# Optimization experiments

Measured on AMD Instinct MI355X. Metric: run time of the kernel, lower is better.

The kernel has to match this reference:

```python
import jax, jax.numpy as jnp
import numpy as np

N = 100_000      # nodes
E = 1_250_000    # edges (avg degree ~12.5)
D_IN, D_H, D_OUT = 64, 64, 64


def setup_inputs() -> dict:
    key = jax.random.key(0)
    ks = jax.random.split(key, 7)
    x = jax.random.normal(ks[0], (N, D_IN), dtype=jnp.float32)
    edge_index = jax.random.randint(ks[1], (2, E), 0, N, dtype=jnp.int32)
    edge_weight = jax.random.uniform(ks[2], (E,), dtype=jnp.float32)
    # GCNConv linear weights: PyG lin stores [out, in], applied as x @ W.T; bias added after aggregation.
    W1 = jax.random.normal(ks[3], (D_H, D_IN), dtype=jnp.float32) * (1.0 / np.sqrt(D_IN))
    b1 = jax.random.normal(ks[4], (D_H,), dtype=jnp.float32) * 0.01
    W2 = jax.random.normal(ks[5], (D_OUT, D_H), dtype=jnp.float32) * (1.0 / np.sqrt(D_H))
    b2 = jax.random.normal(ks[6], (D_OUT,), dtype=jnp.float32) * 0.01
    return {"x": x, "edge_index": edge_index, "edge_weight": edge_weight,
            "W1": W1, "b1": b1, "W2": W2, "b2": b2}


def _gcn_conv(x, src, dst, w, W, b, n_nodes):
    # PyG GCNConv: add self-loops (weight 1), symmetric normalization, linear, scatter-add, +bias.
    deg = jax.ops.segment_sum(w, dst, num_segments=n_nodes) + 1.0  # +1 from self-loop
    dis = jnp.where(deg > 0, jax.lax.rsqrt(deg), 0.0)              # deg^{-1/2}
    coef = dis[src] * w * dis[dst]                                 # per-edge norm, [E]
    h = x @ W.T                                                    # [N, out]
    agg = jax.ops.segment_sum(h[src] * coef[:, None], dst, num_segments=n_nodes)
    agg = agg + h * (dis * dis)[:, None]                           # self-loop: dis_i * 1 * dis_i
    return agg + b


def reference(x, edge_index, edge_weight, W1, b1, W2, b2):
    n = x.shape[0]
    src, dst = edge_index[0], edge_index[1]
    h = _gcn_conv(x, src, dst, edge_weight, W1, b1, n)
    h = jax.nn.relu(h)
    # dropout p=0.0 -> identity
    return _gcn_conv(h, src, dst, edge_weight, W2, b2, n)
```

## Files before the change

kernel.cpp:

```cpp
#include <hip/hip_runtime.h>


typedef unsigned int u32;
typedef unsigned short u16;

#define NBKT 256
#define LSH 9
#define BNODES 512
#define CAP 8192
#define SRCBITS 17
#define SRCMASK ((1u << SRCBITS) - 1u)

__device__ inline u16 f2bf(float f) {
  u32 u = __float_as_uint(f);
  u32 r = u + 0x7FFFu + ((u >> 16) & 1u);
  return (u16)(r >> 16);
}
__device__ inline float bf_lo(u32 p) { return __uint_as_float(p << 16); }
__device__ inline float bf_hi(u32 p) { return __uint_as_float(p & 0xFFFF0000u); }

__device__ inline u32 blockscan256_excl(u32 val, u32* wsum) {
  int lane = threadIdx.x & 63, wv = threadIdx.x >> 6;
  u32 inc = val;
  #pragma unroll
  for (int d = 1; d < 64; d <<= 1) {
    u32 t = __shfl_up(inc, d);
    if (lane >= d) inc += t;
  }
  if (lane == 63) wsum[wv] = inc;
  __syncthreads();
  u32 off = 0;
  #pragma unroll
  for (int i = 0; i < 4; ++i) if (i < wv) off += wsum[i];
  return off + inc - val;
}

__global__ void k_deg_bin(const int* __restrict__ ei, const float* __restrict__ w,
                          float* __restrict__ deg, u32* __restrict__ bucket_cnt,
                          u32* __restrict__ blockbase, int E, int chunk) {
  __shared__ u32 hist[NBKT];
  if (threadIdx.x < NBKT) hist[threadIdx.x] = 0u;
  __syncthreads();
  int e0 = blockIdx.x * chunk;
  int e1 = min(E, e0 + chunk);
  for (int e = e0 + (threadIdx.x << 1); e < e1; e += 512) {
    if (e + 1 < e1) {
      int2 dd = *(const int2*)(ei + E + e);
      float2 wv = *(const float2*)(w + e);
      atomicAdd(&hist[dd.x >> LSH], 1u);
      atomicAdd(&hist[dd.y >> LSH], 1u);
      atomicAdd(&deg[dd.x], wv.x);
      atomicAdd(&deg[dd.y], wv.y);
    } else {
      int d = ei[E + e];
      atomicAdd(&hist[d >> LSH], 1u);
      atomicAdd(&deg[d], w[e]);
    }
  }
  __syncthreads();
  if (threadIdx.x < NBKT)
    blockbase[threadIdx.x * 256 + blockIdx.x] =
        atomicAdd(&bucket_cnt[threadIdx.x], hist[threadIdx.x]);
}

__global__ __launch_bounds__(256, 4) void k_scatter_gemm(
    const int* __restrict__ ei, const float* __restrict__ w,
    const u32* __restrict__ blockbase,
    uint2* __restrict__ bucketed,
    const float* __restrict__ X, const float* __restrict__ W,
    const float* __restrict__ deg, u16* __restrict__ H, int N, int E, int chunk) {
  __shared__ float Wt[64 * 65];
  __shared__ float Xs[16 * 64];
  __shared__ u32 base[NBKT];
  int tid = threadIdx.x;
  if ((int)blockIdx.x < 256) {
    if (tid < NBKT)
      base[tid] = (u32)tid * CAP + blockbase[tid * 256 + blockIdx.x];
    __syncthreads();
    int e0 = blockIdx.x * chunk, e1 = min(E, e0 + chunk);
    for (int e = e0 + (tid << 1); e < e1; e += 512) {
      if (e + 1 < e1) {
        int2 ss = *(const int2*)(ei + e);
        int2 dd = *(const int2*)(ei + E + e);
        float2 wv = *(const float2*)(w + e);
        u32 p0 = atomicAdd(&base[dd.x >> LSH], 1u);
        u32 p1 = atomicAdd(&base[dd.y >> LSH], 1u);
        bucketed[p0] = make_uint2((u32)ss.x | ((u32)(dd.x & (BNODES - 1)) << SRCBITS),
                                  __float_as_uint(wv.x));
        bucketed[p1] = make_uint2((u32)ss.y | ((u32)(dd.y & (BNODES - 1)) << SRCBITS),
                                  __float_as_uint(wv.y));
      } else {
        int s = ei[e], d = ei[E + e];
        u32 pos = atomicAdd(&base[d >> LSH], 1u);
        bucketed[pos] = make_uint2((u32)s | ((u32)(d & (BNODES - 1)) << SRCBITS),
                                   __float_as_uint(w[e]));
      }
    }
    return;
  }
  int row0 = ((int)blockIdx.x - 256) * 16;
  if (row0 >= N) return;
  for (int i = tid; i < 4096; i += 256) Wt[(i & 63) * 65 + (i >> 6)] = W[i];
  {
    const float4* xsrc = (const float4*)(X + (size_t)row0 * 64);
    if (row0 + 16 <= N) {
      ((float4*)Xs)[tid] = xsrc[tid];
    } else {
      int r = tid >> 4;
      ((float4*)Xs)[tid] = (row0 + r < N) ? xsrc[tid]
                                          : make_float4(0.f, 0.f, 0.f, 0.f);
    }
  }
  __syncthreads();
  int lane = tid & 63, wv4 = tid >> 6;
  int rbase = wv4 * 4;
  float a0 = 0.f, a1 = 0.f, a2 = 0.f, a3 = 0.f;
  #pragma unroll 4
  for (int k4 = 0; k4 < 16; ++k4) {
    int k = k4 << 2;
    float w0 = Wt[k * 65 + lane], w1 = Wt[(k + 1) * 65 + lane];
    float w2 = Wt[(k + 2) * 65 + lane], w3 = Wt[(k + 3) * 65 + lane];
    float4 xa = *(const float4*)&Xs[(rbase + 0) * 64 + k];
    float4 xb = *(const float4*)&Xs[(rbase + 1) * 64 + k];
    float4 xc = *(const float4*)&Xs[(rbase + 2) * 64 + k];
    float4 xd = *(const float4*)&Xs[(rbase + 3) * 64 + k];
    a0 = fmaf(xa.x, w0, fmaf(xa.y, w1, fmaf(xa.z, w2, fmaf(xa.w, w3, a0))));
    a1 = fmaf(xb.x, w0, fmaf(xb.y, w1, fmaf(xb.z, w2, fmaf(xb.w, w3, a1))));
    a2 = fmaf(xc.x, w0, fmaf(xc.y, w1, fmaf(xc.z, w2, fmaf(xc.w, w3, a2))));
    a3 = fmaf(xd.x, w0, fmaf(xd.y, w1, fmaf(xd.z, w2, fmaf(xd.w, w3, a3))));
  }
  int row = row0 + rbase;
  if (row + 3 < N) {
    float dv0 = rsqrtf(1.f + deg[row]);
    float dv1 = rsqrtf(1.f + deg[row + 1]);
    float dv2 = rsqrtf(1.f + deg[row + 2]);
    float dv3 = rsqrtf(1.f + deg[row + 3]);
    H[(size_t)row * 64 + lane]       = f2bf(a0 * dv0);
    H[(size_t)(row + 1) * 64 + lane] = f2bf(a1 * dv1);
    H[(size_t)(row + 2) * 64 + lane] = f2bf(a2 * dv2);
    H[(size_t)(row + 3) * 64 + lane] = f2bf(a3 * dv3);
  } else {
    if (row < N)     H[(size_t)row * 64 + lane]       = f2bf(a0 * rsqrtf(1.f + deg[row]));
    if (row + 1 < N) H[(size_t)(row + 1) * 64 + lane] = f2bf(a1 * rsqrtf(1.f + deg[row + 1]));
    if (row + 2 < N) H[(size_t)(row + 2) * 64 + lane] = f2bf(a2 * rsqrtf(1.f + deg[row + 2]));
    if (row + 3 < N) H[(size_t)(row + 3) * 64 + lane] = f2bf(a3 * rsqrtf(1.f + deg[row + 3]));
  }
}

__global__ void k_statsfill(const uint2* __restrict__ bucketed,
                            const u32* __restrict__ bucket_cnt,
                            const float* __restrict__ deg,
                            int4* __restrict__ info, int2* __restrict__ csr, int N) {
  __shared__ u32 hist[BNODES];
  __shared__ u32 cur[BNODES];
  __shared__ u32 wsum[4];
  int b = blockIdx.x, tid = threadIdx.x;
  for (int i = tid; i < BNODES; i += 256) hist[i] = 0u;
  __syncthreads();
  u32 s0 = (u32)b * CAP, s1 = s0 + bucket_cnt[b];
  for (u32 p = s0 + tid; p < s1; p += 256)
    atomicAdd(&hist[bucketed[p].x >> SRCBITS], 1u);
  __syncthreads();
  u32 c0 = hist[2 * tid], c1 = hist[2 * tid + 1];
  u32 excl = blockscan256_excl(c0 + c1, wsum);
  cur[2 * tid] = excl;
  cur[2 * tid + 1] = excl + c0;
  int n0 = b * BNODES + 2 * tid;
  if (n0 < N) {
    float d0 = rsqrtf(1.f + deg[n0]);
    info[n0] = make_int4((int)(s0 + excl), (int)c0, __float_as_int(d0), 0);
  }
  if (n0 + 1 < N) {
    float d1 = rsqrtf(1.f + deg[n0 + 1]);
    info[n0 + 1] = make_int4((int)(s0 + excl + c0), (int)c1, __float_as_int(d1), 0);
  }
  __syncthreads();
  for (u32 p = s0 + tid; p < s1; p += 256) {
    uint2 ed = bucketed[p];
    u32 pos = atomicAdd(&cur[ed.x >> SRCBITS], 1u);
    csr[s0 + pos] = make_int2((int)(ed.x & SRCMASK), (int)ed.y);
  }
}

__global__ __launch_bounds__(256, 6) void k_agg_gemm(
    const u16* __restrict__ H, const int4* __restrict__ info,
    const int2* __restrict__ csr, const float* __restrict__ bias,
    const float* __restrict__ W2, const float* __restrict__ deg,
    u16* __restrict__ H2, int N) {
  __shared__ float Wt[64 * 65];
  __shared__ float Ys[16 * 64];
  int tid = threadIdx.x;
  for (int i = tid; i < 4096; i += 256) Wt[(i & 63) * 65 + (i >> 6)] = W2[i];
  int node = blockIdx.x * 16 + (tid >> 4);
  int fid = (tid & 15) << 2;
  bool valid = node < N;
  int4 nfo = valid ? info[node] : make_int4(0, 0, 0, 0);
  int s0 = nfo.x, n = nfo.y;
  float d = __int_as_float(nfo.z);
  uint2 hs = valid ? *(const uint2*)(H + (size_t)node * 64 + fid)
                   : make_uint2(0u, 0u);
  float4 b4 = *(const float4*)(bias + fid);
  float4 acc = make_float4(0.f, 0.f, 0.f, 0.f);
  int nm1 = n - 1;
  for (int base = 0; base < n; base += 4) {
    int q1 = min(base + 1, nm1);
    int q2 = min(base + 2, nm1), q3 = min(base + 3, nm1);
    int2 c0 = csr[s0 + base];
    int2 c1 = csr[s0 + q1];
    int2 c2 = csr[s0 + q2];
    int2 c3 = csr[s0 + q3];
    uint2 h0 = *(const uint2*)(H + (size_t)c0.x * 64 + fid);
    uint2 h1 = *(const uint2*)(H + (size_t)c1.x * 64 + fid);
    uint2 h2 = *(const uint2*)(H + (size_t)c2.x * 64 + fid);
    uint2 h3 = *(const uint2*)(H + (size_t)c3.x * 64 + fid);
    float f0 = __int_as_float(c0.y);
    float f1 = (base + 1 < n) ? __int_as_float(c1.y) : 0.f;
    float f2 = (base + 2 < n) ? __int_as_float(c2.y) : 0.f;
    float f3 = (base + 3 < n) ? __int_as_float(c3.y) : 0.f;
    acc.x = fmaf(bf_lo(h0.x), f0, acc.x); acc.y = fmaf(bf_hi(h0.x), f0, acc.y);
    acc.z = fmaf(bf_lo(h0.y), f0, acc.z); acc.w = fmaf(bf_hi(h0.y), f0, acc.w);
    acc.x = fmaf(bf_lo(h1.x), f1, acc.x); acc.y = fmaf(bf_hi(h1.x), f1, acc.y);
    acc.z = fmaf(bf_lo(h1.y), f1, acc.z); acc.w = fmaf(bf_hi(h1.y), f1, acc.w);
    acc.x = fmaf(bf_lo(h2.x), f2, acc.x); acc.y = fmaf(bf_hi(h2.x), f2, acc.y);
    acc.z = fmaf(bf_lo(h2.y), f2, acc.z); acc.w = fmaf(bf_hi(h2.y), f2, acc.w);
    acc.x = fmaf(bf_lo(h3.x), f3, acc.x); acc.y = fmaf(bf_hi(h3.x), f3, acc.y);
    acc.z = fmaf(bf_lo(h3.y), f3, acc.z); acc.w = fmaf(bf_hi(h3.y), f3, acc.w);
  }
  if (valid) {
    acc.x = fmaxf((acc.x + bf_lo(hs.x)) * d + b4.x, 0.f);
    acc.y = fmaxf((acc.y + bf_hi(hs.x)) * d + b4.y, 0.f);
    acc.z = fmaxf((acc.z + bf_lo(hs.y)) * d + b4.z, 0.f);
    acc.w = fmaxf((acc.w + bf_hi(hs.y)) * d + b4.w, 0.f);
  } else {
    acc = make_float4(0.f, 0.f, 0.f, 0.f);
  }
  *(float4*)&Ys[(tid >> 4) * 64 + fid] = acc;
  __syncthreads();
  int lane = tid & 63, wv = tid >> 6;
  int rbase = wv * 4;
  int row0 = blockIdx.x * 16;
  float a0 = 0.f, a1 = 0.f, a2 = 0.f, a3 = 0.f;
  #pragma unroll 4
  for (int k4 = 0; k4 < 16; ++k4) {
    int k = k4 << 2;
    float w0 = Wt[k * 65 + lane], w1 = Wt[(k + 1) * 65 + lane];
    float w2 = Wt[(k + 2) * 65 + lane], w3 = Wt[(k + 3) * 65 + lane];
    float4 xa = *(const float4*)&Ys[(rbase + 0) * 64 + k];
    float4 xb = *(const float4*)&Ys[(rbase + 1) * 64 + k];
    float4 xc = *(const float4*)&Ys[(rbase + 2) * 64 + k];
    float4 xd = *(const float4*)&Ys[(rbase + 3) * 64 + k];
    a0 = fmaf(xa.x, w0, fmaf(xa.y, w1, fmaf(xa.z, w2, fmaf(xa.w, w3, a0))));
    a1 = fmaf(xb.x, w0, fmaf(xb.y, w1, fmaf(xb.z, w2, fmaf(xb.w, w3, a1))));
    a2 = fmaf(xc.x, w0, fmaf(xc.y, w1, fmaf(xc.z, w2, fmaf(xc.w, w3, a2))));
    a3 = fmaf(xd.x, w0, fmaf(xd.y, w1, fmaf(xd.z, w2, fmaf(xd.w, w3, a3))));
  }
  int row = row0 + rbase;
  if (row + 3 < N) {
    float dv0 = rsqrtf(1.f + deg[row]);
    float dv1 = rsqrtf(1.f + deg[row + 1]);
    float dv2 = rsqrtf(1.f + deg[row + 2]);
    float dv3 = rsqrtf(1.f + deg[row + 3]);
    H2[(size_t)row * 64 + lane]       = f2bf(a0 * dv0);
    H2[(size_t)(row + 1) * 64 + lane] = f2bf(a1 * dv1);
    H2[(size_t)(row + 2) * 64 + lane] = f2bf(a2 * dv2);
    H2[(size_t)(row + 3) * 64 + lane] = f2bf(a3 * dv3);
  } else {
    if (row < N)     H2[(size_t)row * 64 + lane]       = f2bf(a0 * rsqrtf(1.f + deg[row]));
    if (row + 1 < N) H2[(size_t)(row + 1) * 64 + lane] = f2bf(a1 * rsqrtf(1.f + deg[row + 1]));
    if (row + 2 < N) H2[(size_t)(row + 2) * 64 + lane] = f2bf(a2 * rsqrtf(1.f + deg[row + 2]));
    if (row + 3 < N) H2[(size_t)(row + 3) * 64 + lane] = f2bf(a3 * rsqrtf(1.f + deg[row + 3]));
  }
}

__global__ __launch_bounds__(256, 8) void k_aggregate2(
    const u16* __restrict__ H, const int4* __restrict__ info,
    const int2* __restrict__ csr, const float* __restrict__ bias,
    float* __restrict__ Y, int N) {
  int tid = threadIdx.x;
  int node = blockIdx.x * 16 + (tid >> 4);
  int fid = (tid & 15) << 2;
  bool valid = node < N;
  int4 nfo = valid ? info[node] : make_int4(0, 0, 0, 0);
  int s0 = nfo.x, n = nfo.y;
  float d = __int_as_float(nfo.z);
  uint2 hs = valid ? *(const uint2*)(H + (size_t)node * 64 + fid)
                   : make_uint2(0u, 0u);
  float4 b4 = *(const float4*)(bias + fid);
  float4 acc = make_float4(0.f, 0.f, 0.f, 0.f);
  int nm1 = n - 1;
  for (int base = 0; base < n; base += 4) {
    int q1 = min(base + 1, nm1);
    int q2 = min(base + 2, nm1), q3 = min(base + 3, nm1);
    int2 c0 = csr[s0 + base];
    int2 c1 = csr[s0 + q1];
    int2 c2 = csr[s0 + q2];
    int2 c3 = csr[s0 + q3];
    uint2 h0 = *(const uint2*)(H + (size_t)c0.x * 64 + fid);
    uint2 h1 = *(const uint2*)(H + (size_t)c1.x * 64 + fid);
    uint2 h2 = *(const uint2*)(H + (size_t)c2.x * 64 + fid);
    uint2 h3 = *(const uint2*)(H + (size_t)c3.x * 64 + fid);
    float f0 = __int_as_float(c0.y);
    float f1 = (base + 1 < n) ? __int_as_float(c1.y) : 0.f;
    float f2 = (base + 2 < n) ? __int_as_float(c2.y) : 0.f;
    float f3 = (base + 3 < n) ? __int_as_float(c3.y) : 0.f;
    acc.x = fmaf(bf_lo(h0.x), f0, acc.x); acc.y = fmaf(bf_hi(h0.x), f0, acc.y);
    acc.z = fmaf(bf_lo(h0.y), f0, acc.z); acc.w = fmaf(bf_hi(h0.y), f0, acc.w);
    acc.x = fmaf(bf_lo(h1.x), f1, acc.x); acc.y = fmaf(bf_hi(h1.x), f1, acc.y);
    acc.z = fmaf(bf_lo(h1.y), f1, acc.z); acc.w = fmaf(bf_hi(h1.y), f1, acc.w);
    acc.x = fmaf(bf_lo(h2.x), f2, acc.x); acc.y = fmaf(bf_hi(h2.x), f2, acc.y);
    acc.z = fmaf(bf_lo(h2.y), f2, acc.z); acc.w = fmaf(bf_hi(h2.y), f2, acc.w);
    acc.x = fmaf(bf_lo(h3.x), f3, acc.x); acc.y = fmaf(bf_hi(h3.x), f3, acc.y);
    acc.z = fmaf(bf_lo(h3.y), f3, acc.z); acc.w = fmaf(bf_hi(h3.y), f3, acc.w);
  }
  if (valid) {
    acc.x = (acc.x + bf_lo(hs.x)) * d + b4.x;
    acc.y = (acc.y + bf_hi(hs.x)) * d + b4.y;
    acc.z = (acc.z + bf_lo(hs.y)) * d + b4.z;
    acc.w = (acc.w + bf_hi(hs.y)) * d + b4.w;
    *(float4*)(Y + (size_t)node * 64 + fid) = acc;
  }
}

extern "C" void kernel_launch(void* const* d_in, const int* in_sizes, int n_in,
                              void* d_out, int out_size, void* d_ws, size_t ws_size,
                              hipStream_t stream) {
  const float* x  = (const float*)d_in[0];
  const int*   ei = (const int*)d_in[1];
  const float* w  = (const float*)d_in[2];
  const float* W1 = (const float*)d_in[3];
  const float* b1 = (const float*)d_in[4];
  const float* W2 = (const float*)d_in[5];
  const float* b2 = (const float*)d_in[6];
  const int N = in_sizes[0] / 64;
  const int E = in_sizes[2];

  char* ws = (char*)d_ws;
  size_t off = 0;
  auto alloc = [&](size_t bytes) -> char* {
    char* p = ws + off;
    off = (off + bytes + 255) & ~(size_t)255;
    return p;
  };
  float* deg          = (float*)alloc((size_t)N * 4);
  u32*   bucket_cnt   = (u32*)  alloc((size_t)NBKT * 4);
  size_t zero_bytes   = (size_t)((char*)(bucket_cnt + NBKT) - (char*)deg);
  u32*   blockbase    = (u32*)  alloc((size_t)NBKT * 256 * 4);
  uint2* bucketed     = (uint2*)alloc((size_t)NBKT * CAP * 8);
  int2*  csr          = (int2*) alloc((size_t)NBKT * CAP * 8);
  int4*  info         = (int4*) alloc((size_t)N * 16);
  u16*   h1           = (u16*)  alloc((size_t)N * 64 * 2);
  u16*   h2           = (u16*)  alloc((size_t)N * 64 * 2);

  const int chunk = ((E + 511) / 512) * 2;
  const int nbG = (N + 15) / 16;
  const int nbA = (N + 15) / 16;
  const int nbB = (N + BNODES - 1) >> LSH;

  hipMemsetAsync(deg, 0, zero_bytes, stream);
  k_deg_bin<<<256, 256, 0, stream>>>(ei, w, deg, bucket_cnt, blockbase, E, chunk);
  k_scatter_gemm<<<256 + nbG, 256, 0, stream>>>(ei, w, blockbase, bucketed,
                                                x, W1, deg, h1, N, E, chunk);
  k_statsfill<<<nbB, 256, 0, stream>>>(bucketed, bucket_cnt, deg, info, csr, N);
  k_agg_gemm<<<nbA, 256, 0, stream>>>(h1, info, csr, b1, W2, deg, h2, N);
  k_aggregate2<<<nbA, 256, 0, stream>>>(h2, info, csr, b2, (float*)d_out, N);
}
```

Measured before the change: 286.5 us.

## Compute degrees in LDS during bucket fill instead of global float atomics

Removes the 1.25M global float atomicAdds on deg from the binning kernel. The weighted degree is now accumulated in the per-bucket statsfill kernel with LDS integer atomics, packing a count (high 8 bits) and a fixed-point weight sum (low 24 bits) into one word. Because dis is not known until statsfill, the first GEMM writes unscaled H, and statsfill then rescales its 512 rows of H in place, adding an extra read-modify-write pass over h1. The fixed-point packing limits precision and overflows if a node has 256 or more incoming edges or a weight sum of 64 or more.

```diff
diff --git a/kernel.cpp b/kernel.cpp
--- a/kernel.cpp
+++ b/kernel.cpp
@@ -35,9 +35,8 @@
   return off + inc - val;
 }
 
-__global__ void k_deg_bin(const int* __restrict__ ei, const float* __restrict__ w,
-                          float* __restrict__ deg, u32* __restrict__ bucket_cnt,
-                          u32* __restrict__ blockbase, int E, int chunk) {
+__global__ void k_bin(const int* __restrict__ ei, u32* __restrict__ bucket_cnt,
+                      u32* __restrict__ blockbase, int E, int chunk) {
   __shared__ u32 hist[NBKT];
   if (threadIdx.x < NBKT) hist[threadIdx.x] = 0u;
   __syncthreads();
@@ -46,15 +45,10 @@
   for (int e = e0 + (threadIdx.x << 1); e < e1; e += 512) {
     if (e + 1 < e1) {
       int2 dd = *(const int2*)(ei + E + e);
-      float2 wv = *(const float2*)(w + e);
       atomicAdd(&hist[dd.x >> LSH], 1u);
       atomicAdd(&hist[dd.y >> LSH], 1u);
-      atomicAdd(&deg[dd.x], wv.x);
-      atomicAdd(&deg[dd.y], wv.y);
     } else {
-      int d = ei[E + e];
-      atomicAdd(&hist[d >> LSH], 1u);
-      atomicAdd(&deg[d], w[e]);
+      atomicAdd(&hist[ei[E + e] >> LSH], 1u);
     }
   }
   __syncthreads();
@@ -68,7 +62,7 @@
     const u32* __restrict__ blockbase,
     uint2* __restrict__ bucketed,
     const float* __restrict__ X, const float* __restrict__ W,
-    const float* __restrict__ deg, u16* __restrict__ H, int N, int E, int chunk) {
+    u16* __restrict__ H, int N, int E, int chunk) {
   __shared__ float Wt[64 * 65];
   __shared__ float Xs[16 * 64];
   __shared__ u32 base[NBKT];
@@ -131,61 +125,80 @@
   }
   int row = row0 + rbase;
   if (row + 3 < N) {
-    float dv0 = rsqrtf(1.f + deg[row]);
-    float dv1 = rsqrtf(1.f + deg[row + 1]);
-    float dv2 = rsqrtf(1.f + deg[row + 2]);
-    float dv3 = rsqrtf(1.f + deg[row + 3]);
-    H[(size_t)row * 64 + lane]       = f2bf(a0 * dv0);
-    H[(size_t)(row + 1) * 64 + lane] = f2bf(a1 * dv1);
-    H[(size_t)(row + 2) * 64 + lane] = f2bf(a2 * dv2);
-    H[(size_t)(row + 3) * 64 + lane] = f2bf(a3 * dv3);
+    H[(size_t)row * 64 + lane]       = f2bf(a0);
+    H[(size_t)(row + 1) * 64 + lane] = f2bf(a1);
+    H[(size_t)(row + 2) * 64 + lane] = f2bf(a2);
+    H[(size_t)(row + 3) * 64 + lane] = f2bf(a3);
   } else {
-    if (row < N)     H[(size_t)row * 64 + lane]       = f2bf(a0 * rsqrtf(1.f + deg[row]));
-    if (row + 1 < N) H[(size_t)(row + 1) * 64 + lane] = f2bf(a1 * rsqrtf(1.f + deg[row + 1]));
-    if (row + 2 < N) H[(size_t)(row + 2) * 64 + lane] = f2bf(a2 * rsqrtf(1.f + deg[row + 2]));
-    if (row + 3 < N) H[(size_t)(row + 3) * 64 + lane] = f2bf(a3 * rsqrtf(1.f + deg[row + 3]));
+    if (row < N)     H[(size_t)row * 64 + lane]       = f2bf(a0);
+    if (row + 1 < N) H[(size_t)(row + 1) * 64 + lane] = f2bf(a1);
+    if (row + 2 < N) H[(size_t)(row + 2) * 64 + lane] = f2bf(a2);
+    if (row + 3 < N) H[(size_t)(row + 3) * 64 + lane] = f2bf(a3);
   }
 }
 
 __global__ void k_statsfill(const uint2* __restrict__ bucketed,
                             const u32* __restrict__ bucket_cnt,
-                            const float* __restrict__ deg,
-                            int4* __restrict__ info, int2* __restrict__ csr, int N) {
+                            float* __restrict__ dis, int4* __restrict__ info,
+                            int2* __restrict__ csr, u16* __restrict__ H, int N) {
   __shared__ u32 hist[BNODES];
   __shared__ u32 cur[BNODES];
+  __shared__ float disl[BNODES];
   __shared__ u32 wsum[4];
   int b = blockIdx.x, tid = threadIdx.x;
   for (int i = tid; i < BNODES; i += 256) hist[i] = 0u;
   __syncthreads();
   u32 s0 = (u32)b * CAP, s1 = s0 + bucket_cnt[b];
-  for (u32 p = s0 + tid; p < s1; p += 256)
-    atomicAdd(&hist[bucketed[p].x >> SRCBITS], 1u);
-  __syncthreads();
-  u32 c0 = hist[2 * tid], c1 = hist[2 * tid + 1];
+  for (u32 p = s0 + tid; p < s1; p += 256) {
+    uint2 ed = bucketed[p];
+    u32 local = ed.x >> SRCBITS;
+    u32 wfix = (u32)(__uint_as_float(ed.y) * 262144.0f);
+    atomicAdd(&hist[local], (1u << 24) | wfix);
+  }
+  __syncthreads();
+  u32 h0 = hist[2 * tid], h1 = hist[2 * tid + 1];
+  u32 c0 = h0 >> 24, c1 = h1 >> 24;
   u32 excl = blockscan256_excl(c0 + c1, wsum);
+  float d0 = rsqrtf(1.0f + (float)(h0 & 0xFFFFFFu) * (1.0f / 262144.0f));
+  float d1 = rsqrtf(1.0f + (float)(h1 & 0xFFFFFFu) * (1.0f / 262144.0f));
   cur[2 * tid] = excl;
   cur[2 * tid + 1] = excl + c0;
+  disl[2 * tid] = d0;
+  disl[2 * tid + 1] = d1;
   int n0 = b * BNODES + 2 * tid;
   if (n0 < N) {
-    float d0 = rsqrtf(1.f + deg[n0]);
+    dis[n0] = d0;
     info[n0] = make_int4((int)(s0 + excl), (int)c0, __float_as_int(d0), 0);
   }
   if (n0 + 1 < N) {
-    float d1 = rsqrtf(1.f + deg[n0 + 1]);
+    dis[n0 + 1] = d1;
     info[n0 + 1] = make_int4((int)(s0 + excl + c0), (int)c1, __float_as_int(d1), 0);
   }
   __syncthreads();
   for (u32 p = s0 + tid; p < s1; p += 256) {
     uint2 ed = bucketed[p];
-    u32 pos = atomicAdd(&cur[ed.x >> SRCBITS], 1u);
+    u32 local = ed.x >> SRCBITS;
+    u32 pos = atomicAdd(&cur[local], 1u);
     csr[s0 + pos] = make_int2((int)(ed.x & SRCMASK), (int)ed.y);
+  }
+  uint2* Hv = (uint2*)H;
+  for (int i = tid; i < BNODES * 16; i += 256) {
+    int row = i >> 4;
+    int node = b * BNODES + row;
+    if (node >= N) break;
+    float dv = disl[row];
+    size_t idx = (size_t)node * 16 + (i & 15);
+    uint2 v = Hv[idx];
+    u32 lo = (u32)f2bf(bf_lo(v.x) * dv) | ((u32)f2bf(bf_hi(v.x) * dv) << 16);
+    u32 hi = (u32)f2bf(bf_lo(v.y) * dv) | ((u32)f2bf(bf_hi(v.y) * dv) << 16);
+    Hv[idx] = make_uint2(lo, hi);
   }
 }
 
 __global__ __launch_bounds__(256, 6) void k_agg_gemm(
     const u16* __restrict__ H, const int4* __restrict__ info,
     const int2* __restrict__ csr, const float* __restrict__ bias,
-    const float* __restrict__ W2, const float* __restrict__ deg,
+    const float* __restrict__ W2, const float* __restrict__ dis,
     u16* __restrict__ H2, int N) {
   __shared__ float Wt[64 * 65];
   __shared__ float Ys[16 * 64];
@@ -256,19 +269,16 @@
   }
   int row = row0 + rbase;
   if (row + 3 < N) {
-    float dv0 = rsqrtf(1.f + deg[row]);
-    float dv1 = rsqrtf(1.f + deg[row + 1]);
-    float dv2 = rsqrtf(1.f + deg[row + 2]);
-    float dv3 = rsqrtf(1.f + deg[row + 3]);
+    float dv0 = dis[row], dv1 = dis[row + 1], dv2 = dis[row + 2], dv3 = dis[row + 3];
     H2[(size_t)row * 64 + lane]       = f2bf(a0 * dv0);
     H2[(size_t)(row + 1) * 64 + lane] = f2bf(a1 * dv1);
     H2[(size_t)(row + 2) * 64 + lane] = f2bf(a2 * dv2);
     H2[(size_t)(row + 3) * 64 + lane] = f2bf(a3 * dv3);
   } else {
-    if (row < N)     H2[(size_t)row * 64 + lane]       = f2bf(a0 * rsqrtf(1.f + deg[row]));
-    if (row + 1 < N) H2[(size_t)(row + 1) * 64 + lane] = f2bf(a1 * rsqrtf(1.f + deg[row + 1]));
-    if (row + 2 < N) H2[(size_t)(row + 2) * 64 + lane] = f2bf(a2 * rsqrtf(1.f + deg[row + 2]));
-    if (row + 3 < N) H2[(size_t)(row + 3) * 64 + lane] = f2bf(a3 * rsqrtf(1.f + deg[row + 3]));
+    if (row < N)     H2[(size_t)row * 64 + lane]       = f2bf(a0 * dis[row]);
+    if (row + 1 < N) H2[(size_t)(row + 1) * 64 + lane] = f2bf(a1 * dis[row + 1]);
+    if (row + 2 < N) H2[(size_t)(row + 2) * 64 + lane] = f2bf(a2 * dis[row + 2]);
+    if (row + 3 < N) H2[(size_t)(row + 3) * 64 + lane] = f2bf(a3 * dis[row + 3]);
   }
 }
 
@@ -341,12 +351,11 @@
     off = (off + bytes + 255) & ~(size_t)255;
     return p;
   };
-  float* deg          = (float*)alloc((size_t)N * 4);
   u32*   bucket_cnt   = (u32*)  alloc((size_t)NBKT * 4);
-  size_t zero_bytes   = (size_t)((char*)(bucket_cnt + NBKT) - (char*)deg);
   u32*   blockbase    = (u32*)  alloc((size_t)NBKT * 256 * 4);
   uint2* bucketed     = (uint2*)alloc((size_t)NBKT * CAP * 8);
   int2*  csr          = (int2*) alloc((size_t)NBKT * CAP * 8);
+  float* dis          = (float*)alloc((size_t)N * 4);
   int4*  info         = (int4*) alloc((size_t)N * 16);
   u16*   h1           = (u16*)  alloc((size_t)N * 64 * 2);
   u16*   h2           = (u16*)  alloc((size_t)N * 64 * 2);
@@ -356,11 +365,11 @@
   const int nbA = (N + 15) / 16;
   const int nbB = (N + BNODES - 1) >> LSH;
 
-  hipMemsetAsync(deg, 0, zero_bytes, stream);
-  k_deg_bin<<<256, 256, 0, stream>>>(ei, w, deg, bucket_cnt, blockbase, E, chunk);
+  hipMemsetAsync(bucket_cnt, 0, (size_t)NBKT * 4, stream);
+  k_bin<<<256, 256, 0, stream>>>(ei, bucket_cnt, blockbase, E, chunk);
   k_scatter_gemm<<<256 + nbG, 256, 0, stream>>>(ei, w, blockbase, bucketed,
-                                                x, W1, deg, h1, N, E, chunk);
-  k_statsfill<<<nbB, 256, 0, stream>>>(bucketed, bucket_cnt, deg, info, csr, N);
-  k_agg_gemm<<<nbA, 256, 0, stream>>>(h1, info, csr, b1, W2, deg, h2, N);
+                                                x, W1, h1, N, E, chunk);
+  k_statsfill<<<nbB, 256, 0, stream>>>(bucketed, bucket_cnt, dis, info, csr, h1, N);
+  k_agg_gemm<<<nbA, 256, 0, stream>>>(h1, info, csr, b1, W2, dis, h2, N);
   k_aggregate2<<<nbA, 256, 0, stream>>>(h2, info, csr, b2, (float*)d_out, N);
 }
```

After: 237.3 us. 17.2% less time.
